# Optimization experiments

Hardware: AMD Instinct MI355X
Metric: run time of the kernel (lower is better)

Reference implementation:

```python
import jax, jax.numpy as jnp
import numpy as np

B, T, K = 8, 2048, 4          # lattices, nodes per lattice, incoming edges per node
E = T * K                     # edges per lattice
D = 256                       # input_dim
H = 256                       # hidden_dim (== input_dim, required by node_h assignment)


def setup_inputs() -> dict:
    key = jax.random.key(0)
    k1, k2, k3, k4, k5 = jax.random.split(key, 5)
    edge_input = jax.random.normal(k1, (B, E, D), dtype=jnp.float32)
    weight_ih = jax.random.normal(k2, (D, 4 * H), dtype=jnp.float32) * (1.0 / np.sqrt(D))
    weight_hh = jax.random.normal(k3, (H, 4 * H), dtype=jnp.float32) * (1.0 / np.sqrt(H))
    bias = jax.random.normal(k4, (4 * H,), dtype=jnp.float32) * 0.02
    prev_idx = jax.random.randint(k5, (T, K), 0, E, dtype=jnp.int32)  # prevs[step]
    return {"edge_input": edge_input, "weight_ih": weight_ih,
            "weight_hh": weight_hh, "bias": bias, "prev_idx": prev_idx}


def reference(edge_input, weight_ih, weight_hh, bias, prev_idx):
    # Faithful to the source: node_h/node_c read by EdgeCell at step t are row t,
    # which is only written at the END of iteration t -> always zeros when read.
    # Therefore node_hh = 0 @ weight_hh + bias = bias, and c0 = 0, and every
    # edge's gates depend only on its own input. (weight_hh thus has no effect,
    # exactly as in the original numerics.)
    pre = jnp.einsum('bed,dh->beh', edge_input, weight_ih) + bias  # [B,E,4H]
    i, f, g, o = jnp.split(pre, 4, axis=-1)
    # c = sigmoid(f)*c0 + sigmoid(i)*tanh(g), with c0 == 0
    edge_c = jax.nn.sigmoid(i) * jnp.tanh(g)                       # [B,E,H]
    # source bug kept verbatim: h = o.sigmoid() * o.tanh()
    edge_h = jax.nn.sigmoid(o) * jnp.tanh(o)                       # [B,E,H]
    # node state = mean over incoming (prev) edges
    node_h = edge_h[:, prev_idx, :].mean(axis=2)                   # [B,T,H]
    node_c = edge_c[:, prev_idx, :].mean(axis=2)                   # [B,T,H]
    return node_h, node_c, edge_h, edge_c
```

## Files before the change

### kernel.cpp

```cpp
#include <hip/hip_runtime.h>
#include <hip/hip_bf16.h>
#include <stdint.h>

typedef __attribute__((ext_vector_type(8))) __bf16 bf16x8;
typedef __attribute__((ext_vector_type(4))) float f32x4;
typedef __attribute__((ext_vector_type(4))) uint32_t u32x4;

#define B_SZ 8
#define E_SZ 8192
#define T_SZ 2048
#define D_SZ 256
#define H_SZ 256
#define NP   768

#define BM 128
#define BN 192
#define BK 64
#define NTHR 512
#define NWG  2048
#define TILE_BYTES ((BM + BN) * BK * 2)

#define NODE_H_OFF 0
#define NODE_C_OFF (B_SZ*T_SZ*H_SZ)
#define EDGE_H_OFF (2*B_SZ*T_SZ*H_SZ)
#define EDGE_C_OFF (2*B_SZ*T_SZ*H_SZ + B_SZ*E_SZ*H_SZ)

__device__ __forceinline__ uint32_t pk_bf16(float a, float b) {
    uint32_t ua = __float_as_uint(a);
    uint32_t ub = __float_as_uint(b);
    ua += 0x7fffu + ((ua >> 16) & 1u);
    ub += 0x7fffu + ((ub >> 16) & 1u);
    return (ua >> 16) | (ub & 0xffff0000u);
}

__global__ void wcvt_kernel(const float* __restrict__ W, const float* __restrict__ bias,
                            uint16_t* __restrict__ Wt, float* __restrict__ biasp) {
    int id = blockIdx.x * 256 + threadIdx.x;
    if (id < 256 * 768) {
        int k = id / 768;
        int q = id - k * 768;
        int col = (q < 256) ? q : (q + 256);
        int s = q >> 8;
        int j = q & 255;
        int np = 48 * (j >> 4) + 16 * s + (j & 15);
        uint32_t ua = __float_as_uint(W[k * 1024 + col]);
        ua += 0x7fffu + ((ua >> 16) & 1u);
        Wt[np * 256 + k] = (uint16_t)(ua >> 16);
        if (k == 0) biasp[np] = bias[col];
    }
}

__launch_bounds__(NTHR, 4)
__global__ void gemm_act_kernel(const float* __restrict__ A,
                                const uint16_t* __restrict__ Wt,
                                const float* __restrict__ biasp,
                                float* __restrict__ out) {
    __shared__ __align__(16) char smem[2 * TILE_BYTES];

    const int tid  = threadIdx.x;
    const int bid  = blockIdx.x;
    const int wg   = (bid & 7) * (NWG / 8) + (bid >> 3);
    const int mb   = wg >> 2;
    const int nb   = wg & 3;
    const int m0   = mb * BM;
    const int n0   = nb * BN;

    const int wid  = tid >> 6;
    const int lane = tid & 63;
    const int wm   = wid >> 2;
    const int wn   = wid & 3;
    const int l15  = lane & 15;
    const int lq   = lane >> 4;

    const int aid0  = tid;
    const int aid1  = NTHR + tid;
    const int arow0 = aid0 >> 3, ac0 = (aid0 & 7) * 16;
    const int arow1 = aid1 >> 3, ac1 = (aid1 & 7) * 16;
    const int asw0  = ac0 ^ ((arow0 & 7) << 4);
    const int asw1  = ac1 ^ ((arow1 & 7) << 4);

    f32x4 acc[4][3];
    #pragma unroll
    for (int mf = 0; mf < 4; ++mf)
        #pragma unroll
        for (int nf = 0; nf < 3; ++nf)
            acc[mf][nf] = (f32x4){0.f, 0.f, 0.f, 0.f};

    {
        char* As = smem;
        char* Bs = smem + BM * BK * 2;
        const float* ga0 = A + (size_t)(m0 + arow0) * D_SZ + (ac0 >> 1);
        const float* ga1 = A + (size_t)(m0 + arow1) * D_SZ + (ac1 >> 1);
        f32x4 x0 = *(const f32x4*)ga0, x1 = *(const f32x4*)(ga0 + 4);
        f32x4 x2 = *(const f32x4*)ga1, x3 = *(const f32x4*)(ga1 + 4);
        #pragma unroll
        for (int r2 = 0; r2 < 3; ++r2) {
            int p   = (r2 * NTHR + tid) * 16;
            int row = p >> 7;
            int csw = (p & 127) ^ ((row & 7) << 4);
            const uint16_t* g = Wt + (n0 + row) * 256 + (csw >> 1);
            __builtin_amdgcn_global_load_lds(
                (const __attribute__((address_space(1))) uint32_t*)g,
                (__attribute__((address_space(3))) uint32_t*)(Bs + p), 16, 0, 0);
        }
        u32x4 v0 = { pk_bf16(x0.x,x0.y), pk_bf16(x0.z,x0.w), pk_bf16(x1.x,x1.y), pk_bf16(x1.z,x1.w) };
        u32x4 v1 = { pk_bf16(x2.x,x2.y), pk_bf16(x2.z,x2.w), pk_bf16(x3.x,x3.y), pk_bf16(x3.z,x3.w) };
        *(u32x4*)(As + arow0 * 128 + asw0) = v0;
        *(u32x4*)(As + arow1 * 128 + asw1) = v1;
    }
    __syncthreads();

    #pragma unroll
    for (int kt = 0; kt < 4; ++kt) {
        char* AsC = smem + (kt & 1) * TILE_BYTES;
        char* BsC = AsC + BM * BK * 2;
        char* AsN = smem + ((kt + 1) & 1) * TILE_BYTES;
        char* BsN = AsN + BM * BK * 2;

        f32x4 x0, x1, x2, x3;
        if (kt < 3) {
            const int k0n = (kt + 1) * BK;
            const float* ga0 = A + (size_t)(m0 + arow0) * D_SZ + k0n + (ac0 >> 1);
            const float* ga1 = A + (size_t)(m0 + arow1) * D_SZ + k0n + (ac1 >> 1);
            x0 = *(const f32x4*)ga0; x1 = *(const f32x4*)(ga0 + 4);
            x2 = *(const f32x4*)ga1; x3 = *(const f32x4*)(ga1 + 4);
            #pragma unroll
            for (int r2 = 0; r2 < 3; ++r2) {
                int p   = (r2 * NTHR + tid) * 16;
                int row = p >> 7;
                int csw = (p & 127) ^ ((row & 7) << 4);
                const uint16_t* g = Wt + (n0 + row) * 256 + k0n + (csw >> 1);
                __builtin_amdgcn_global_load_lds(
                    (const __attribute__((address_space(1))) uint32_t*)g,
                    (__attribute__((address_space(3))) uint32_t*)(BsN + p), 16, 0, 0);
            }
        }

        #pragma unroll
        for (int kk = 0; kk < 2; ++kk) {
            const int kb = kk * 64 + lq * 16;
            bf16x8 af[4], bfr[3];
            #pragma unroll
            for (int mf = 0; mf < 4; ++mf) {
                int row = wm * 64 + mf * 16 + l15;
                af[mf] = *(const bf16x8*)(AsC + row * 128 + (kb ^ ((row & 7) << 4)));
            }
            #pragma unroll
            for (int nf = 0; nf < 3; ++nf) {
                int row = wn * 48 + nf * 16 + l15;
                bfr[nf] = *(const bf16x8*)(BsC + row * 128 + (kb ^ ((row & 7) << 4)));
            }
            #pragma unroll
            for (int mf = 0; mf < 4; ++mf)
                #pragma unroll
                for (int nf = 0; nf < 3; ++nf)
                    acc[mf][nf] = __builtin_amdgcn_mfma_f32_16x16x32_bf16(
                        af[mf], bfr[nf], acc[mf][nf], 0, 0, 0);
        }

        if (kt < 3) {
            u32x4 v0 = { pk_bf16(x0.x,x0.y), pk_bf16(x0.z,x0.w), pk_bf16(x1.x,x1.y), pk_bf16(x1.z,x1.w) };
            u32x4 v1 = { pk_bf16(x2.x,x2.y), pk_bf16(x2.z,x2.w), pk_bf16(x3.x,x3.y), pk_bf16(x3.z,x3.w) };
            *(u32x4*)(AsN + arow0 * 128 + asw0) = v0;
            *(u32x4*)(AsN + arow1 * 128 + asw1) = v1;
            __syncthreads();
        }
    }

    const float L2E = 1.44269504088896340736f;
    const int jj = (nb * 4 + wn) * 16 + l15;
    const int bb = n0 + wn * 48 + l15;
    const float bi = biasp[bb];
    const float bg = biasp[bb + 16];
    const float bo = biasp[bb + 32];
    float* __restrict__ eh = out + EDGE_H_OFF;
    float* __restrict__ ec = out + EDGE_C_OFF;
    #pragma unroll
    for (int mf = 0; mf < 4; ++mf) {
        const int mbase = m0 + wm * 64 + mf * 16 + lq * 4;
        #pragma unroll
        for (int r = 0; r < 4; ++r) {
            const size_t m = (size_t)(mbase + r);
            float pi = acc[mf][0][r] + bi;
            float pg = acc[mf][1][r] + bg;
            float po = acc[mf][2][r] + bo;
            float ei = __builtin_amdgcn_exp2f(-L2E * pi);
            float eg = __builtin_amdgcn_exp2f(-2.f * L2E * pg);
            float eo = __builtin_amdgcn_exp2f(-L2E * po);
            float c  = (1.f - eg) * __builtin_amdgcn_rcpf((1.f + ei) * (1.f + eg));
            float h  = (1.f - eo) * __builtin_amdgcn_rcpf(1.f + eo * eo);
            eh[m * H_SZ + jj] = h;
            ec[m * H_SZ + jj] = c;
        }
    }
}

__global__ void node_mean_kernel(const int* __restrict__ prev,
                                 const float* __restrict__ outr,
                                 float* __restrict__ out) {
    int gid  = blockIdx.x * 4 + (threadIdx.x >> 6);
    int lane = threadIdx.x & 63;
    int b = gid >> 11;
    int t = gid & 2047;
    const float* eh = outr + EDGE_H_OFF + (size_t)b * E_SZ * H_SZ;
    const float* ec = outr + EDGE_C_OFF + (size_t)b * E_SZ * H_SZ;
    f32x4 hs = (f32x4){0.f,0.f,0.f,0.f};
    f32x4 cs = (f32x4){0.f,0.f,0.f,0.f};
    #pragma unroll
    for (int k = 0; k < 4; ++k) {
        int e = prev[t * 4 + k];
        hs += *(const f32x4*)(eh + (size_t)e * H_SZ + lane * 4);
        cs += *(const f32x4*)(ec + (size_t)e * H_SZ + lane * 4);
    }
    hs *= 0.25f; cs *= 0.25f;
    size_t o = (size_t)(b * T_SZ + t) * H_SZ + lane * 4;
    *(f32x4*)(out + NODE_H_OFF + o) = hs;
    *(f32x4*)(out + NODE_C_OFF + o) = cs;
}

extern "C" void kernel_launch(void* const* d_in, const int* in_sizes, int n_in,
                              void* d_out, int out_size, void* d_ws, size_t ws_size,
                              hipStream_t stream) {
    const float* edge_input = (const float*)d_in[0];
    const float* weight_ih  = (const float*)d_in[1];
    const float* bias       = (const float*)d_in[3];
    const int*   prev_idx   = (const int*)d_in[4];
    float* out = (float*)d_out;

    uint16_t* Wt    = (uint16_t*)d_ws;
    float*    biasp = (float*)((char*)d_ws + NP * 256 * 2);

    wcvt_kernel<<<(256 * 768 + 255) / 256, 256, 0, stream>>>(weight_ih, bias, Wt, biasp);
    gemm_act_kernel<<<NWG, NTHR, 0, stream>>>(edge_input, Wt, biasp, out);
    node_mean_kernel<<<(B_SZ * T_SZ) / 4, 256, 0, stream>>>(prev_idx, out, out);
}
```

Baseline: 77.85 us.

## Prefetch A tiles two stages ahead with explicit waitcnt and barriers

The GEMM main loop now loads the fp32 A tile two K-steps ahead into a double-buffered register array, rather than one step ahead. It replaces __syncthreads with hand-placed s_waitcnt vmcnt/lgkmcnt plus s_barrier, and uses sched_barrier to fix instruction order. The aim is to hide global load latency behind MFMA work. The explicit vmcnt counts depend on how the compiler emits and orders the loads, so they risk being wrong, and the extra live registers may lower occupancy. The node-mean kernel also loads its four prev indices as one vector.

```diff
diff --git a/kernel.cpp b/kernel.cpp
--- a/kernel.cpp
+++ b/kernel.cpp
@@ -4,6 +4,7 @@
 
 typedef __attribute__((ext_vector_type(8))) __bf16 bf16x8;
 typedef __attribute__((ext_vector_type(4))) float f32x4;
+typedef __attribute__((ext_vector_type(4))) int   i32x4;
 typedef __attribute__((ext_vector_type(4))) uint32_t u32x4;
 
 #define B_SZ 8
@@ -16,6 +17,7 @@
 #define BM 128
 #define BN 192
 #define BK 64
+#define KT 4
 #define NTHR 512
 #define NWG  2048
 #define TILE_BYTES ((BM + BN) * BK * 2)
@@ -78,6 +80,43 @@
     const int arow1 = aid1 >> 3, ac1 = (aid1 & 7) * 16;
     const int asw0  = ac0 ^ ((arow0 & 7) << 4);
     const int asw1  = ac1 ^ ((arow1 & 7) << 4);
+    const float* ga0base = A + (size_t)(m0 + arow0) * D_SZ + (ac0 >> 1);
+    const float* ga1base = A + (size_t)(m0 + arow1) * D_SZ + (ac1 >> 1);
+
+    f32x4 xs[2][2][2];
+
+    xs[0][0][0] = *(const f32x4*)(ga0base);
+    xs[0][0][1] = *(const f32x4*)(ga0base + 4);
+    xs[0][1][0] = *(const f32x4*)(ga1base);
+    xs[0][1][1] = *(const f32x4*)(ga1base + 4);
+    __builtin_amdgcn_sched_barrier(0);
+    #pragma unroll
+    for (int r2 = 0; r2 < 3; ++r2) {
+        int p   = (r2 * NTHR + tid) * 16;
+        int row = p >> 7;
+        int csw = (p & 127) ^ ((row & 7) << 4);
+        const uint16_t* g = Wt + (n0 + row) * 256 + (csw >> 1);
+        __builtin_amdgcn_global_load_lds(
+            (const __attribute__((address_space(1))) uint32_t*)g,
+            (__attribute__((address_space(3))) uint32_t*)(smem + BM * BK * 2 + p), 16, 0, 0);
+    }
+    __builtin_amdgcn_sched_barrier(0);
+    xs[1][0][0] = *(const f32x4*)(ga0base + BK);
+    xs[1][0][1] = *(const f32x4*)(ga0base + BK + 4);
+    xs[1][1][0] = *(const f32x4*)(ga1base + BK);
+    xs[1][1][1] = *(const f32x4*)(ga1base + BK + 4);
+    __builtin_amdgcn_sched_barrier(0);
+    {
+        u32x4 v0 = { pk_bf16(xs[0][0][0].x,xs[0][0][0].y), pk_bf16(xs[0][0][0].z,xs[0][0][0].w),
+                     pk_bf16(xs[0][0][1].x,xs[0][0][1].y), pk_bf16(xs[0][0][1].z,xs[0][0][1].w) };
+        u32x4 v1 = { pk_bf16(xs[0][1][0].x,xs[0][1][0].y), pk_bf16(xs[0][1][0].z,xs[0][1][0].w),
+                     pk_bf16(xs[0][1][1].x,xs[0][1][1].y), pk_bf16(xs[0][1][1].z,xs[0][1][1].w) };
+        *(u32x4*)(smem + arow0 * 128 + asw0) = v0;
+        *(u32x4*)(smem + arow1 * 128 + asw1) = v1;
+    }
+    asm volatile("s_waitcnt lgkmcnt(0)" ::: "memory");
+    asm volatile("s_waitcnt vmcnt(4)" ::: "memory");
+    __builtin_amdgcn_s_barrier();
 
     f32x4 acc[4][3];
     #pragma unroll
@@ -86,44 +125,15 @@
         for (int nf = 0; nf < 3; ++nf)
             acc[mf][nf] = (f32x4){0.f, 0.f, 0.f, 0.f};
 
-    {
-        char* As = smem;
-        char* Bs = smem + BM * BK * 2;
-        const float* ga0 = A + (size_t)(m0 + arow0) * D_SZ + (ac0 >> 1);
-        const float* ga1 = A + (size_t)(m0 + arow1) * D_SZ + (ac1 >> 1);
-        f32x4 x0 = *(const f32x4*)ga0, x1 = *(const f32x4*)(ga0 + 4);
-        f32x4 x2 = *(const f32x4*)ga1, x3 = *(const f32x4*)(ga1 + 4);
-        #pragma unroll
-        for (int r2 = 0; r2 < 3; ++r2) {
-            int p   = (r2 * NTHR + tid) * 16;
-            int row = p >> 7;
-            int csw = (p & 127) ^ ((row & 7) << 4);
-            const uint16_t* g = Wt + (n0 + row) * 256 + (csw >> 1);
-            __builtin_amdgcn_global_load_lds(
-                (const __attribute__((address_space(1))) uint32_t*)g,
-                (__attribute__((address_space(3))) uint32_t*)(Bs + p), 16, 0, 0);
-        }
-        u32x4 v0 = { pk_bf16(x0.x,x0.y), pk_bf16(x0.z,x0.w), pk_bf16(x1.x,x1.y), pk_bf16(x1.z,x1.w) };
-        u32x4 v1 = { pk_bf16(x2.x,x2.y), pk_bf16(x2.z,x2.w), pk_bf16(x3.x,x3.y), pk_bf16(x3.z,x3.w) };
-        *(u32x4*)(As + arow0 * 128 + asw0) = v0;
-        *(u32x4*)(As + arow1 * 128 + asw1) = v1;
-    }
-    __syncthreads();
-
-    #pragma unroll
-    for (int kt = 0; kt < 4; ++kt) {
+    #pragma unroll
+    for (int kt = 0; kt < KT; ++kt) {
         char* AsC = smem + (kt & 1) * TILE_BYTES;
         char* BsC = AsC + BM * BK * 2;
         char* AsN = smem + ((kt + 1) & 1) * TILE_BYTES;
         char* BsN = AsN + BM * BK * 2;
 
-        f32x4 x0, x1, x2, x3;
-        if (kt < 3) {
+        if (kt < KT - 1) {
             const int k0n = (kt + 1) * BK;
-            const float* ga0 = A + (size_t)(m0 + arow0) * D_SZ + k0n + (ac0 >> 1);
-            const float* ga1 = A + (size_t)(m0 + arow1) * D_SZ + k0n + (ac1 >> 1);
-            x0 = *(const f32x4*)ga0; x1 = *(const f32x4*)(ga0 + 4);
-            x2 = *(const f32x4*)ga1; x3 = *(const f32x4*)(ga1 + 4);
             #pragma unroll
             for (int r2 = 0; r2 < 3; ++r2) {
                 int p   = (r2 * NTHR + tid) * 16;
@@ -135,6 +145,15 @@
                     (__attribute__((address_space(3))) uint32_t*)(BsN + p), 16, 0, 0);
             }
         }
+        __builtin_amdgcn_sched_barrier(0);
+        if (kt < KT - 2) {
+            const int k0n2 = (kt + 2) * BK;
+            xs[kt & 1][0][0] = *(const f32x4*)(ga0base + k0n2);
+            xs[kt & 1][0][1] = *(const f32x4*)(ga0base + k0n2 + 4);
+            xs[kt & 1][1][0] = *(const f32x4*)(ga1base + k0n2);
+            xs[kt & 1][1][1] = *(const f32x4*)(ga1base + k0n2 + 4);
+        }
+        __builtin_amdgcn_sched_barrier(0);
 
         #pragma unroll
         for (int kk = 0; kk < 2; ++kk) {
@@ -158,12 +177,21 @@
                         af[mf], bfr[nf], acc[mf][nf], 0, 0, 0);
         }
 
-        if (kt < 3) {
-            u32x4 v0 = { pk_bf16(x0.x,x0.y), pk_bf16(x0.z,x0.w), pk_bf16(x1.x,x1.y), pk_bf16(x1.z,x1.w) };
-            u32x4 v1 = { pk_bf16(x2.x,x2.y), pk_bf16(x2.z,x2.w), pk_bf16(x3.x,x3.y), pk_bf16(x3.z,x3.w) };
+        if (kt < KT - 1) {
+            const int sl = (kt + 1) & 1;
+            u32x4 v0 = { pk_bf16(xs[sl][0][0].x,xs[sl][0][0].y), pk_bf16(xs[sl][0][0].z,xs[sl][0][0].w),
+                         pk_bf16(xs[sl][0][1].x,xs[sl][0][1].y), pk_bf16(xs[sl][0][1].z,xs[sl][0][1].w) };
+            u32x4 v1 = { pk_bf16(xs[sl][1][0].x,xs[sl][1][0].y), pk_bf16(xs[sl][1][0].z,xs[sl][1][0].w),
+                         pk_bf16(xs[sl][1][1].x,xs[sl][1][1].y), pk_bf16(xs[sl][1][1].z,xs[sl][1][1].w) };
             *(u32x4*)(AsN + arow0 * 128 + asw0) = v0;
             *(u32x4*)(AsN + arow1 * 128 + asw1) = v1;
-            __syncthreads();
+            asm volatile("s_waitcnt lgkmcnt(0)" ::: "memory");
+            if (kt < KT - 2) {
+                asm volatile("s_waitcnt vmcnt(4)" ::: "memory");
+            } else {
+                asm volatile("s_waitcnt vmcnt(0)" ::: "memory");
+            }
+            __builtin_amdgcn_s_barrier();
         }
     }
 
@@ -204,13 +232,14 @@
     int t = gid & 2047;
     const float* eh = outr + EDGE_H_OFF + (size_t)b * E_SZ * H_SZ;
     const float* ec = outr + EDGE_C_OFF + (size_t)b * E_SZ * H_SZ;
+    i32x4 e4 = *(const i32x4*)(prev + t * 4);
     f32x4 hs = (f32x4){0.f,0.f,0.f,0.f};
     f32x4 cs = (f32x4){0.f,0.f,0.f,0.f};
     #pragma unroll
     for (int k = 0; k < 4; ++k) {
-        int e = prev[t * 4 + k];
-        hs += *(const f32x4*)(eh + (size_t)e * H_SZ + lane * 4);
-        cs += *(const f32x4*)(ec + (size_t)e * H_SZ + lane * 4);
+        size_t off = (size_t)e4[k] * H_SZ + lane * 4;
+        hs += *(const f32x4*)(eh + off);
+        cs += *(const f32x4*)(ec + off);
     }
     hs *= 0.25f; cs *= 0.25f;
     size_t o = (size_t)(b * T_SZ + t) * H_SZ + lane * 4;
```

Result: slower. 135.5 us (+74.0%).
